# Performance work log

Measured on AMD Instinct MI355X. Metric: run time of the kernel, lower is better.

The kernel has to match this reference:

```python
import jax, jax.numpy as jnp
import numpy as np

N = 8192        # agents (single node type VEHICLE)
K = 15          # max_Nnode - 1 neighbors per node
E = N * K       # edges
FT = 12         # prediction horizon steps
SD = 4          # state dim (x, y, vx, vy)
ID = 2          # input dim (ax, ay)
ZD = 8          # latent z dim
HE = 256        # history_enc_dim
EE = 128        # edge_enc_dim
OH = 256        # obs_lstm_hidden_dim
GH = 256        # guide_RNN_hidden_dim
FH = 256        # FC_hidden_dim
AD = 16         # att_internal_dim
DT = 0.25
SCALE = 1.0     # input_scale


def setup_inputs() -> dict:
    ks = jax.random.split(jax.random.key(0), 40)
    f = lambda i, s: jax.random.normal(ks[i], s, jnp.float32)
    w = lambda i, s: 0.05 * jax.random.normal(ks[i], s, jnp.float32)
    inp = dict(
        x_last=f(0, (N, SD)), x_st_last=f(1, (N, SD)), hist_enc=f(2, (N, HE)),
        z=f(3, (N, ZD)),
        node_size=jax.random.uniform(ks[4], (N, 2), jnp.float32, 1.0, 3.0),
        W_h0=w(5, (SD, OH)), b_h0=w(6, (OH,)), W_c0=w(7, (SD, OH)), b_c0=w(8, (OH,)),
        W_gh=w(9, (HE + ZD, GH)), b_gh=w(10, (GH,)),
        W_gru_ih=w(11, (HE + ZD, 3 * GH)), W_gru_hh=w(12, (GH, 3 * GH)),
        b_gru_ih=w(13, (3 * GH,)), b_gru_hh=w(14, (3 * GH,)),
        W_proj=w(15, (GH, 2)), b_proj=w(16, (2,)),
        W_att1=w(17, (EE, AD)), W_att2=w(18, (SD, AD)), v_att=w(19, (AD,)),
        W_lstm_ih=w(20, (EE, 4 * OH)), W_lstm_hh=w(21, (OH, 4 * OH)),
        b_lstm_ih=w(22, (4 * OH,)), b_lstm_hh=w(23, (4 * OH,)),
        W_e1=w(24, (SD + 4, FH)), b_e1=w(25, (FH,)), W_e2=w(26, (FH, EE)), b_e2=w(27, (EE,)),
        W_a1=w(28, (OH + ZD + SD + 4, FH)), b_a1=w(29, (FH,)),
        W_a2=w(30, (FH, ID)), b_a2=w(31, (ID,)),
    )
    # edge k is the j-th neighbor of node k // K; index 0 in the enc table is the pad row
    inp["edge_idx1"] = jnp.repeat(jnp.arange(N), K)
    inp["edge_idx2"] = jax.random.randint(ks[32], (E,), 0, N)
    inp["node_obs_idx"] = (jnp.arange(E) + 1).reshape(N, K)
    inp["ft"] = FT
    return inp


def _dyn(s, u):
    # double-integrator: s = [x, y, vx, vy], u = [ax, ay]
    pos = s[:, :2] + s[:, 2:4] * DT + 0.5 * u * DT * DT
    vel = s[:, 2:4] + u * DT
    return jnp.concatenate([pos, vel], -1)


def _forward(x_last, x_st_last, hist_enc, z, node_size,
             W_h0, b_h0, W_c0, b_c0, W_gh, b_gh, W_gru_ih, W_gru_hh, b_gru_ih, b_gru_hh,
             W_proj, b_proj, W_att1, W_att2, v_att, W_lstm_ih, W_lstm_hh, b_lstm_ih, b_lstm_hh,
             W_e1, b_e1, W_e2, b_e2, W_a1, b_a1, W_a2, b_a2,
             edge_idx1, edge_idx2, node_obs_idx, ft):
    n = x_last.shape[0]
    ee = W_e2.shape[1]
    # ---- guide GRU: desired trajectory [ft, N, 2] ----
    xz = jnp.concatenate([hist_enc, z], -1)
    h0g = xz @ W_gh + b_gh
    gi = xz @ W_gru_ih + b_gru_ih  # input is constant over time (xz repeated)
    ir, iz, inn = jnp.split(gi, 3, -1)

    def gru_step(h, _):
        hr, hz, hn = jnp.split(h @ W_gru_hh + b_gru_hh, 3, -1)
        r = jax.nn.sigmoid(ir + hr)
        u = jax.nn.sigmoid(iz + hz)
        nh = (1.0 - u) * jnp.tanh(inn + r * hn) + u * h
        return nh, nh

    _, hs = jax.lax.scan(gru_step, h0g, None, length=ft)
    des = hs @ W_proj + b_proj                       # [ft, N, 2]
    des_next = jnp.concatenate([des[1:], des[-1:]], 0)
    des_prev = jnp.concatenate([jnp.zeros_like(des[:1]), des[:-1]], 0)
    first = jnp.zeros((ft,), jnp.float32).at[0].set(1.0)

    # ---- obs LSTM initial state ----
    h0 = x_st_last @ W_h0 + b_h0
    c0 = x_st_last @ W_c0 + b_c0

    size1 = node_size[edge_idx1]
    size2 = node_size[edge_idx2]
    rad = 0.5 * (jnp.linalg.norm(size1, axis=-1) + jnp.linalg.norm(size2, axis=-1))

    def step(carry, xs):
        prev, prev_st, h, c, terr, ccost = carry
        des_t, des_n, des_p, fst = xs
        # edge gather + collision cost + edge encoding
        s1 = prev[edge_idx1]
        s2 = prev[edge_idx2]
        dist = jnp.linalg.norm(s1[:, :2] - s2[:, :2], axis=-1)
        ccost = ccost + jnp.sum(jax.nn.relu(rad - dist))
        feat = jnp.concatenate([s2 - s1, size1, size2], -1)          # [E, SD+4]
        enc = jax.nn.relu(feat @ W_e1 + b_e1) @ W_e2 + b_e2          # [E, EE]
        enc_all = jnp.concatenate([jnp.zeros((1, ee), enc.dtype), enc], 0)
        obs = enc_all[node_obs_idx]                                   # [N, K, EE]
        # relative state (t==0 uses standardized history directly)
        m = 1.0 - fst
        rel = prev_st - m * x_st_last
        rel = jnp.concatenate([rel[:, :2] - m * des_p, rel[:, 2:]], -1)
        terr = terr + jnp.linalg.norm(rel[:, :2]) / n
        next_wp = des_t - prev_st[:, :2]
        next_wp2 = des_n - prev_st[:, :2]
        # additive attention over neighbors
        scores = jnp.tanh(obs @ W_att1 + (rel @ W_att2)[:, None, :]) @ v_att   # [N, K]
        att = jax.nn.softmax(scores, axis=-1)
        ctx = jnp.einsum('nk,nkd->nd', att, obs)
        # LSTM cell (torch gate order i, f, g, o)
        gates = ctx @ W_lstm_ih + b_lstm_ih + h @ W_lstm_hh + b_lstm_hh
        g_i, g_f, g_g, g_o = jnp.split(gates, 4, -1)
        c = jax.nn.sigmoid(g_f) * c + jax.nn.sigmoid(g_i) * jnp.tanh(g_g)
        h = jax.nn.sigmoid(g_o) * jnp.tanh(c)
        # action net + dynamics rollout
        a_in = jnp.concatenate([h, z, rel, next_wp, next_wp2], -1)   # [N, OH+ZD+SD+4]
        u = SCALE * jnp.tanh(jax.nn.relu(a_in @ W_a1 + b_a1) @ W_a2 + b_a2)
        nxt = _dyn(prev, u)
        nxt_st = _dyn(prev_st, u)
        return (nxt, nxt_st, h, c, terr, ccost), (nxt, u)

    zero = jnp.zeros((), jnp.float32)
    init = (x_last, x_st_last, h0, c0, zero, zero)
    (_, _, _, _, terr, ccost), (state_pred, input_pred) = jax.lax.scan(
        step, init, (des, des_next, des_prev, first))
    return state_pred, input_pred, terr, ccost


def reference(x_last, x_st_last, hist_enc, z, node_size,
              W_h0, b_h0, W_c0, b_c0, W_gh, b_gh, W_gru_ih, W_gru_hh, b_gru_ih, b_gru_hh,
              W_proj, b_proj, W_att1, W_att2, v_att, W_lstm_ih, W_lstm_hh, b_lstm_ih, b_lstm_hh,
              W_e1, b_e1, W_e2, b_e2, W_a1, b_a1, W_a2, b_a2,
              edge_idx1, edge_idx2, node_obs_idx, ft):
    return _forward(x_last, x_st_last, hist_enc, z, node_size,
                    W_h0, b_h0, W_c0, b_c0, W_gh, b_gh, W_gru_ih, W_gru_hh, b_gru_ih, b_gru_hh,
                    W_proj, b_proj, W_att1, W_att2, v_att, W_lstm_ih, W_lstm_hh, b_lstm_ih, b_lstm_hh,
                    W_e1, b_e1, W_e2, b_e2, W_a1, b_a1, W_a2, b_a2,
                    edge_idx1, edge_idx2, node_obs_idx, ft)
```

## Files before the change

### kernel.cpp

```cpp
#include <hip/hip_runtime.h>

#define DEVI __device__ __forceinline__

constexpr int N_  = 8192;
constexpr int K_  = 15;
constexpr int E_  = N_ * K_;
constexpr int FTS = 12;
constexpr float DT_ = 0.25f;

typedef __attribute__((ext_vector_type(8))) short short8x;
typedef __attribute__((ext_vector_type(4))) float float4x;

union U8 { unsigned int u[4]; short8x v; };

DEVI float sigf(float x) { return 1.0f / (1.0f + __expf(-x)); }
DEVI float tanhf_fast(float x) { float e = __expf(2.f * x); return 1.f - 2.f / (e + 1.f); }
DEVI unsigned int f2u(float x) { union { float f; unsigned int u; } c; c.f = x; return c.u; }
DEVI float u2f(unsigned int x) { union { unsigned int u; float f; } c; c.u = x; return c.f; }

DEVI void split8(const float* __restrict__ s, short8x& hi8, short8x& lo8) {
  U8 ph, pl;
#pragma unroll
  for (int p = 0; p < 4; p++) {
    float a0 = s[2*p], a1 = s[2*p+1];
    unsigned int u0 = f2u(a0), u1 = f2u(a1);
    unsigned int h0 = u0 & 0xFFFF0000u, h1 = u1 & 0xFFFF0000u;
    ph.u[p] = (u0 >> 16) | h1;
    float l0 = a0 - u2f(h0), l1 = a1 - u2f(h1);
    pl.u[p] = (f2u(l0) >> 16) | (f2u(l1) & 0xFFFF0000u);
  }
  hi8 = ph.v; lo8 = pl.v;
}

__global__ void k_zero(float* ss) {
  ss[blockIdx.x * 256 + threadIdx.x] = 0.f;
}

__global__ __launch_bounds__(256) void k_init_des(const float* __restrict__ b_proj,
                                                  float* __restrict__ des) {
  int i = blockIdx.x * 256 + threadIdx.x;
  des[i*2]     = b_proj[0];
  des[i*2 + 1] = b_proj[1];
}

__global__ __launch_bounds__(256) void k_edge_static(
    const int* __restrict__ e1, const int* __restrict__ e2,
    const float* __restrict__ nsize, float* __restrict__ rad, float* __restrict__ szf)
{
  int e = blockIdx.x * 256 + threadIdx.x;
  if (e >= E_) return;
  int i1 = e1[e], i2 = e2[e];
  float s1x = nsize[i1*2+0], s1y = nsize[i1*2+1];
  float s2x = nsize[i2*2+0], s2y = nsize[i2*2+1];
  rad[e] = 0.5f * (sqrtf(s1x*s1x + s1y*s1y) + sqrtf(s2x*s2x + s2y*s2y));
  *(float4*)&szf[e*4] = make_float4(s1x, s1y, s2x, s2y);
}

__global__ __launch_bounds__(256) void k_prep_hi(
    const float* __restrict__ W, unsigned short* __restrict__ out)
{
  int t = blockIdx.x * 256 + threadIdx.x;
  int fid = t >> 6, L = t & 63;
  int ks = fid >> 3, nt = fid & 7;
  int k0 = ks * 32 + (L >> 4) * 8;
  int n  = nt * 16 + (L & 15);
  unsigned int hi[4];
#pragma unroll
  for (int p = 0; p < 4; p++) {
    float w0 = W[(size_t)(k0 + 2*p) * 128 + n];
    float w1 = W[(size_t)(k0 + 2*p + 1) * 128 + n];
    hi[p] = (f2u(w0) >> 16) | (f2u(w1) & 0xFFFF0000u);
  }
  *(uint4*)(out + (size_t)fid * 512 + (size_t)L * 8) = make_uint4(hi[0], hi[1], hi[2], hi[3]);
}

__global__ __launch_bounds__(256) void k_prep1(
    const float* __restrict__ WA, const float* __restrict__ WB,
    int mode, int split, int wA, int wB, int Ktot, int NT, int nfrag,
    unsigned short* __restrict__ out)
{
  int t = blockIdx.x * 256 + threadIdx.x;
  int fid = t >> 6, L = t & 63;
  if (fid >= nfrag) return;
  int ks = fid / NT, nt = fid % NT;
  int k0 = ks * 32 + (L >> 4) * 8;
  int n  = nt * 16 + (L & 15);
  unsigned int hi[4];
#pragma unroll
  for (int p = 0; p < 4; p++) {
    float w0 = 0.f, w1 = 0.f;
    int ka = k0 + 2*p, kb = ka + 1;
    if (mode == 0) {
      if (ka < Ktot) w0 = (ka < split) ? WA[(size_t)ka*wA + n] : WB[(size_t)(ka-split)*wB + n];
      if (kb < Ktot) w1 = (kb < split) ? WA[(size_t)kb*wA + n] : WB[(size_t)(kb-split)*wB + n];
    } else {
      if (ka < Ktot) w0 = (n < split) ? WA[(size_t)ka*wA + n] : WB[(size_t)ka*wB + (n-split)];
      if (kb < Ktot) w1 = (n < split) ? WA[(size_t)kb*wA + n] : WB[(size_t)kb*wB + (n-split)];
    }
    hi[p] = (f2u(w0) >> 16) | (f2u(w1) & 0xFFFF0000u);
  }
  *(uint4*)(out + (size_t)fid * 512 + (size_t)L * 8) = make_uint4(hi[0], hi[1], hi[2], hi[3]);
}

__global__ __launch_bounds__(256) void k_xz_mfma(
    const float* __restrict__ hist, const float* __restrict__ z,
    const unsigned short* __restrict__ wB,
    const float* __restrict__ b_gh, const float* __restrict__ b_gih,
    float* __restrict__ gh0, float* __restrict__ gi)
{
  __shared__ __align__(16) float Abuf[2][64][36];
  const int tid = threadIdx.x;
  const int w = tid >> 6, lane = tid & 63;
  const int m = lane & 15, q = lane >> 4;
  const int n0 = blockIdx.x * 64;
  const int r_ = tid >> 2, c_ = (tid & 3) * 8;
  float4x acc[16];
#pragma unroll
  for (int tl = 0; tl < 16; tl++) acc[tl] = (float4x){0.f,0.f,0.f,0.f};

  auto LD = [&](int ks, float4& v0, float4& v1) {
    int kk = ks*32 + c_;
    int n = n0 + r_;
    if (kk < 256) {
      v0 = *(const float4*)&hist[(size_t)n*256 + kk];
      v1 = *(const float4*)&hist[(size_t)n*256 + kk + 4];
    } else if (kk == 256) {
      v0 = *(const float4*)&z[n*8];
      v1 = *(const float4*)&z[n*8 + 4];
    } else {
      v0 = make_float4(0,0,0,0); v1 = v0;
    }
  };
  {
    float4 v0, v1; LD(0, v0, v1);
    *(float4*)&Abuf[0][r_][c_]     = v0;
    *(float4*)&Abuf[0][r_][c_ + 4] = v1;
  }
  __syncthreads();
  for (int ks = 0; ks < 9; ks++) {
    float4 v0, v1;
    if (ks < 8) LD(ks + 1, v0, v1);
    short8x aHi, aLo;
    split8(&Abuf[ks & 1][w*16 + m][q*8], aHi, aLo);
#pragma unroll
    for (int tl = 0; tl < 16; tl++) {
      int nt = blockIdx.y*16 + tl;
      size_t off = (size_t)(ks*64 + nt) * 512 + (size_t)lane*8;
      short8x bh = *(const short8x*)(wB + off);
      acc[tl] = __builtin_amdgcn_mfma_f32_16x16x32_bf16(aLo, bh, acc[tl], 0, 0, 0);
      acc[tl] = __builtin_amdgcn_mfma_f32_16x16x32_bf16(aHi, bh, acc[tl], 0, 0, 0);
    }
    if (ks < 8) {
      *(float4*)&Abuf[(ks+1) & 1][r_][c_]     = v0;
      *(float4*)&Abuf[(ks+1) & 1][r_][c_ + 4] = v1;
      __syncthreads();
    }
  }
#pragma unroll
  for (int tl = 0; tl < 16; tl++) {
    int col = (blockIdx.y*16 + tl)*16 + m;
    float bias = (col < 256) ? b_gh[col] : b_gih[col - 256];
#pragma unroll
    for (int i = 0; i < 4; i++) {
      int n = n0 + w*16 + q*4 + i;
      float v = acc[tl][i] + bias;
      if (col < 256) gh0[(size_t)n*256 + col] = v;
      else           gi[(size_t)n*768 + col - 256] = v;
    }
  }
}

DEVI void gru_core(int tid, int n0, int j0,
                   const float* __restrict__ h_in, const unsigned short* __restrict__ wB,
                   const float* __restrict__ b_hh, const float* __restrict__ gi,
                   const float* __restrict__ W_proj, float* __restrict__ des_t,
                   float* __restrict__ h_out)
{
  const int w = tid >> 6, lane = tid & 63;
  const int m = lane & 15, q = lane >> 4;
  const float* __restrict__ hrow = h_in + (size_t)(n0 + w*16 + m) * 256 + q*8;
  float4x acc[12];
#pragma unroll
  for (int tl = 0; tl < 12; tl++) acc[tl] = (float4x){0.f,0.f,0.f,0.f};

  for (int ks = 0; ks < 8; ks++) {
    float a8[8];
    {
      float4 v0 = *(const float4*)(hrow + ks*32);
      float4 v1 = *(const float4*)(hrow + ks*32 + 4);
      a8[0]=v0.x; a8[1]=v0.y; a8[2]=v0.z; a8[3]=v0.w;
      a8[4]=v1.x; a8[5]=v1.y; a8[6]=v1.z; a8[7]=v1.w;
    }
    short8x aHi, aLo;
    split8(a8, aHi, aLo);
#pragma unroll
    for (int tl = 0; tl < 12; tl++) {
      int g = tl >> 2, jt = tl & 3;
      int nt = g*16 + (j0 >> 4) + jt;
      size_t off = (size_t)(ks*48 + nt) * 512 + (size_t)lane*8;
      short8x bh = *(const short8x*)(wB + off);
      acc[tl] = __builtin_amdgcn_mfma_f32_16x16x32_bf16(aLo, bh, acc[tl], 0, 0, 0);
      acc[tl] = __builtin_amdgcn_mfma_f32_16x16x32_bf16(aHi, bh, acc[tl], 0, 0, 0);
    }
  }
  float pd0[4] = {0,0,0,0}, pd1[4] = {0,0,0,0};
#pragma unroll
  for (int jt = 0; jt < 4; jt++) {
    int j = j0 + jt*16 + m;
    float br = b_hh[j], bz = b_hh[256 + j], bn = b_hh[512 + j];
    float wp0 = W_proj[j*2], wp1 = W_proj[j*2 + 1];
#pragma unroll
    for (int i = 0; i < 4; i++) {
      int n = n0 + w*16 + q*4 + i;
      float ir  = gi[(size_t)n*768 + j];
      float iz  = gi[(size_t)n*768 + 256 + j];
      float inn = gi[(size_t)n*768 + 512 + j];
      float hold = h_in[(size_t)n*256 + j];
      float r = sigf(ir + acc[0*4 + jt][i] + br);
      float u = sigf(iz + acc[1*4 + jt][i] + bz);
      float nh = (1.f - u) * tanhf_fast(inn + r * (acc[2*4 + jt][i] + bn)) + u * hold;
      h_out[(size_t)n*256 + j] = nh;
      pd0[i] += nh * wp0;
      pd1[i] += nh * wp1;
    }
  }
#pragma unroll
  for (int off = 1; off < 16; off <<= 1) {
#pragma unroll
    for (int i = 0; i < 4; i++) {
      pd0[i] += __shfl_xor(pd0[i], off);
      pd1[i] += __shfl_xor(pd1[i], off);
    }
  }
  if (m == 0) {
#pragma unroll
    for (int i = 0; i < 4; i++) {
      int n = n0 + w*16 + q*4 + i;
      atomicAdd(&des_t[n*2],     pd0[i]);
      atomicAdd(&des_t[n*2 + 1], pd1[i]);
    }
  }
}

__global__ __launch_bounds__(256) void k_gru_mfma(
    const float* __restrict__ h_in, const unsigned short* __restrict__ wB,
    const float* __restrict__ b_hh, const float* __restrict__ gi,
    const float* __restrict__ W_proj, float* __restrict__ des_t,
    float* __restrict__ h_out)
{
  gru_core(threadIdx.x, blockIdx.x * 64, blockIdx.y * 64,
           h_in, wB, b_hh, gi, W_proj, des_t, h_out);
}

__global__ __launch_bounds__(256) void k_lstm_mfma(
    const float* __restrict__ ctxg, const float* __restrict__ h_in,
    const unsigned short* __restrict__ wB,
    const float* __restrict__ b_ih, const float* __restrict__ b_hh,
    float* __restrict__ c_st, float* __restrict__ h_out)
{
  __shared__ __align__(16) float Abuf[2][64][36];
  const int tid = threadIdx.x;
  const int w = tid >> 6, lane = tid & 63;
  const int m = lane & 15, q = lane >> 4;
  const int n0 = blockIdx.x * 64;
  const int j0 = blockIdx.y * 32;
  const int r_ = tid >> 2, c_ = (tid & 3) * 8;
  float4x acc[8];
#pragma unroll
  for (int tl = 0; tl < 8; tl++) acc[tl] = (float4x){0.f,0.f,0.f,0.f};

  auto LD = [&](int ks, float4& v0, float4& v1) {
    int kk = ks*32 + c_;
    int n = n0 + r_;
    if (kk < 128) {
      v0 = *(const float4*)&ctxg[(size_t)n*128 + kk];
      v1 = *(const float4*)&ctxg[(size_t)n*128 + kk + 4];
    } else {
      v0 = *(const float4*)&h_in[(size_t)n*256 + kk - 128];
      v1 = *(const float4*)&h_in[(size_t)n*256 + kk - 124];
    }
  };
  {
    float4 v0, v1; LD(0, v0, v1);
    *(float4*)&Abuf[0][r_][c_]     = v0;
    *(float4*)&Abuf[0][r_][c_ + 4] = v1;
  }
  __syncthreads();
  for (int ks = 0; ks < 12; ks++) {
    float4 v0, v1;
    if (ks < 11) LD(ks + 1, v0, v1);
    short8x aHi, aLo;
    split8(&Abuf[ks & 1][w*16 + m][q*8], aHi, aLo);
#pragma unroll
    for (int tl = 0; tl < 8; tl++) {
      int g = tl >> 1, jt = tl & 1;
      int nt = g*16 + (j0 >> 4) + jt;
      size_t off = (size_t)(ks*64 + nt) * 512 + (size_t)lane*8;
      short8x bh = *(const short8x*)(wB + off);
      acc[tl] = __builtin_amdgcn_mfma_f32_16x16x32_bf16(aLo, bh, acc[tl], 0, 0, 0);
      acc[tl] = __builtin_amdgcn_mfma_f32_16x16x32_bf16(aHi, bh, acc[tl], 0, 0, 0);
    }
    if (ks < 11) {
      *(float4*)&Abuf[(ks+1) & 1][r_][c_]     = v0;
      *(float4*)&Abuf[(ks+1) & 1][r_][c_ + 4] = v1;
      __syncthreads();
    }
  }
#pragma unroll
  for (int jt = 0; jt < 2; jt++) {
    int j = j0 + jt*16 + m;
    float bi = b_ih[j]       + b_hh[j];
    float bf = b_ih[256 + j] + b_hh[256 + j];
    float bg = b_ih[512 + j] + b_hh[512 + j];
    float bo = b_ih[768 + j] + b_hh[768 + j];
#pragma unroll
    for (int i = 0; i < 4; i++) {
      int n = n0 + w*16 + q*4 + i;
      float g_i = sigf(acc[0*2 + jt][i] + bi);
      float g_f = sigf(acc[1*2 + jt][i] + bf);
      float g_g = tanhf_fast(acc[2*2 + jt][i] + bg);
      float g_o = sigf(acc[3*2 + jt][i] + bo);
      float cv = g_f * c_st[(size_t)n*256 + j] + g_i * g_g;
      c_st[(size_t)n*256 + j] = cv;
      h_out[(size_t)n*256 + j] = g_o * tanhf_fast(cv);
    }
  }
}

__global__ __launch_bounds__(256) void k_action_mfma(
    const float* __restrict__ h, const float* __restrict__ z,
    const float* __restrict__ rel, const float* __restrict__ nwp, const float* __restrict__ nwp2,
    const unsigned short* __restrict__ wB, const float* __restrict__ b_a1,
    const float* __restrict__ W_a2, const float* __restrict__ b_a2,
    float* __restrict__ prev, float* __restrict__ prev_st,
    float* __restrict__ outS, float* __restrict__ outU)
{
  __shared__ __align__(16) float Abuf[2][32][36];
  __shared__ float sm_p[2][16][2];
  const int tid = threadIdx.x;
  const int w = tid >> 6, lane = tid & 63;
  const int m = lane & 15, q = lane >> 4;
  const int ng = w >> 1, hh = w & 1;
  const int n0 = blockIdx.x * 32;
  const int r_ = tid >> 3, c_ = (tid & 7) * 4;
  float4x acc[8];
#pragma unroll
  for (int j = 0; j < 8; j++) acc[j] = (float4x){0.f,0.f,0.f,0.f};

  auto LD = [&](int ks) -> float4 {
    int kk = ks*32 + c_;
    int n = n0 + r_;
    float4 v;
    if (kk < 256)       v = *(const float4*)&h[(size_t)n*256 + kk];
    else if (kk == 256) v = *(const float4*)&z[n*8];
    else if (kk == 260) v = *(const float4*)&z[n*8 + 4];
    else if (kk == 264) v = *(const float4*)&rel[n*4];
    else if (kk == 268) {
      float2 w1 = *(const float2*)&nwp[n*2];
      float2 w2 = *(const float2*)&nwp2[n*2];
      v = make_float4(w1.x, w1.y, w2.x, w2.y);
    } else v = make_float4(0,0,0,0);
    return v;
  };
  {
    float4 v = LD(0);
    *(float4*)&Abuf[0][r_][c_] = v;
  }
  __syncthreads();
  for (int ks = 0; ks < 9; ks++) {
    float4 v;
    if (ks < 8) v = LD(ks + 1);
    short8x aHi, aLo;
    split8(&Abuf[ks & 1][ng*16 + m][q*8], aHi, aLo);
#pragma unroll
    for (int j = 0; j < 8; j++) {
      int tl = hh*8 + j;
      size_t off = (size_t)(ks*16 + tl) * 512 + (size_t)lane*8;
      short8x bh = *(const short8x*)(wB + off);
      acc[j] = __builtin_amdgcn_mfma_f32_16x16x32_bf16(aLo, bh, acc[j], 0, 0, 0);
      acc[j] = __builtin_amdgcn_mfma_f32_16x16x32_bf16(aHi, bh, acc[j], 0, 0, 0);
    }
    if (ks < 8) {
      *(float4*)&Abuf[(ks+1) & 1][r_][c_] = v;
      __syncthreads();
    }
  }
  float p0[4] = {0,0,0,0}, p1[4] = {0,0,0,0};
#pragma unroll
  for (int j = 0; j < 8; j++) {
    int col = (hh*8 + j)*16 + m;
    float ba = b_a1[col];
    float2 w2 = *(const float2*)&W_a2[col*2];
#pragma unroll
    for (int i = 0; i < 4; i++) {
      float hv = fmaxf(acc[j][i] + ba, 0.f);
      p0[i] += hv * w2.x;
      p1[i] += hv * w2.y;
    }
  }
#pragma unroll
  for (int off = 1; off < 16; off <<= 1) {
#pragma unroll
    for (int i = 0; i < 4; i++) {
      p0[i] += __shfl_xor(p0[i], off);
      p1[i] += __shfl_xor(p1[i], off);
    }
  }
  if (hh == 1 && m == 0) {
#pragma unroll
    for (int i = 0; i < 4; i++) {
      sm_p[ng][q*4 + i][0] = p0[i];
      sm_p[ng][q*4 + i][1] = p1[i];
    }
  }
  __syncthreads();
  if (hh == 0 && m == 0) {
    float ba0 = b_a2[0], ba1 = b_a2[1];
    const float hd = 0.5f * DT_ * DT_;
#pragma unroll
    for (int i = 0; i < 4; i++) {
      int n = n0 + ng*16 + q*4 + i;
      float ux = tanhf_fast(p0[i] + sm_p[ng][q*4 + i][0] + ba0);
      float uy = tanhf_fast(p1[i] + sm_p[ng][q*4 + i][1] + ba1);
      float4 pv = *(const float4*)&prev[n*4];
      float4 ps = *(const float4*)&prev_st[n*4];
      float4 npv, nps;
      npv.x = pv.x + pv.z*DT_ + ux*hd;
      npv.y = pv.y + pv.w*DT_ + uy*hd;
      npv.z = pv.z + ux*DT_;
      npv.w = pv.w + uy*DT_;
      nps.x = ps.x + ps.z*DT_ + ux*hd;
      nps.y = ps.y + ps.w*DT_ + uy*hd;
      nps.z = ps.z + ux*DT_;
      nps.w = ps.w + uy*DT_;
      *(float4*)&prev[n*4] = npv;
      *(float4*)&prev_st[n*4] = nps;
      *(float4*)&outS[(size_t)n*4] = npv;
      outU[n*2]     = ux;
      outU[n*2 + 1] = uy;
    }
  }
}

__global__ __launch_bounds__(256) void k_init_hc(
    const float* __restrict__ x_last, const float* __restrict__ x_st_last,
    const float* __restrict__ W_h0, const float* __restrict__ b_h0,
    const float* __restrict__ W_c0, const float* __restrict__ b_c0,
    float* __restrict__ h, float* __restrict__ c,
    float* __restrict__ prev, float* __restrict__ prev_st)
{
  const int n = blockIdx.x;
  const int j = threadIdx.x;
  float x0 = x_st_last[n*4], x1 = x_st_last[n*4+1], x2 = x_st_last[n*4+2], x3 = x_st_last[n*4+3];
  h[(size_t)n*256 + j] = b_h0[j] + x0*W_h0[j] + x1*W_h0[256+j] + x2*W_h0[512+j] + x3*W_h0[768+j];
  c[(size_t)n*256 + j] = b_c0[j] + x0*W_c0[j] + x1*W_c0[256+j] + x2*W_c0[512+j] + x3*W_c0[768+j];
  if (j < 4) prev[n*4 + j] = x_last[n*4 + j];
  else if (j < 8) prev_st[n*4 + (j-4)] = x_st_last[n*4 + (j-4)];
}

__global__ __launch_bounds__(256, 4) void k_edge_gru(
    const float* __restrict__ prev, const float* __restrict__ prev_st,
    const float* __restrict__ x_st_last,
    const float* __restrict__ szf, const float* __restrict__ rad,
    const int* __restrict__ nobs, const int* __restrict__ e1, const int* __restrict__ e2,
    const float* __restrict__ W_e1, const float* __restrict__ b_e1,
    const unsigned short* __restrict__ wsB, const float* __restrict__ b_e2,
    const unsigned short* __restrict__ wattA, const float* __restrict__ W_att2,
    const float* __restrict__ v_att,
    const float* __restrict__ des_p, const float* __restrict__ des_t,
    const float* __restrict__ des_n,
    float* __restrict__ relg, float* __restrict__ nwp, float* __restrict__ nwp2,
    float* __restrict__ ctx, float* __restrict__ ss_t, float* __restrict__ cc,
    const float* __restrict__ g_hin, const unsigned short* __restrict__ wBg,
    const float* __restrict__ b_ghh, const float* __restrict__ gi,
    const float* __restrict__ W_proj, float* __restrict__ des_g,
    float* __restrict__ g_hout, int gru_on)
{
  __shared__ __align__(16) float smem[4776];
  const int tid = threadIdx.x;
  const int bid = blockIdx.x;

  if ((bid % 5) == 4) {
    if (!gru_on) return;
    int b = bid / 5;
    gru_core(tid, (b & 127) * 64, (b >> 7) * 64,
             g_hin, wBg, b_ghh, gi, W_proj, des_g, g_hout);
    return;
  }
  const int eb = bid - (bid + 1) / 5;

  float* sm_stage = smem;
  float* sm_feats = smem + 4096;
  float* sm_flags = smem + 4608;
  float* sm_relv  = smem + 4672;
  float* sm_watt2 = smem + 4688;
  float* sm_vatt  = smem + 4752;
  float* sm_red   = smem + 4768;

  const int n0  = eb * 4;
  const int slot = (eb & 15) << 4;
  const int lane = tid & 63;
  const int g    = tid >> 6;
  const int q = lane >> 4, m = lane & 15;

  if (tid >= 176 && tid < 192) sm_vatt[tid - 176] = v_att[tid - 176];
  if (tid >= 192) sm_watt2[tid - 192] = W_att2[tid - 192];

  if (tid < 64) {
    float v = 0.f;
    if (tid < 60) {
      int gg = tid / 15, k = tid % 15;
      int idx = nobs[(n0 + gg) * 15 + k];
      float f[8] = {0,0,0,0,0,0,0,0};
      float fl = 0.f;
      if (idx > 0) {
        int e = idx - 1;
        int i1 = e1[e], i2 = e2[e];
#pragma unroll
        for (int d = 0; d < 4; d++) f[d] = prev[i2*4 + d] - prev[i1*4 + d];
        float4 sz = *(const float4*)&szf[(size_t)e*4];
        f[4] = sz.x; f[5] = sz.y; f[6] = sz.z; f[7] = sz.w;
        fl = 1.f;
        float dist = sqrtf(f[0]*f[0] + f[1]*f[1]);
        v = fmaxf(rad[e] - dist, 0.f);
      }
#pragma unroll
      for (int d = 0; d < 8; d++) sm_feats[(gg*16 + k)*8 + d] = f[d];
      sm_flags[gg*16 + k] = fl;
    } else {
      int gg = tid - 60;
#pragma unroll
      for (int d = 0; d < 8; d++) sm_feats[(gg*16 + 15)*8 + d] = 0.f;
      sm_flags[gg*16 + 15] = 0.f;
    }
#pragma unroll
    for (int off = 32; off; off >>= 1) v += __shfl_down(v, off);
    if (tid == 0) atomicAdd(cc + slot, v);
  } else if (tid < 68) {
    int gg = tid - 64;
    int n = n0 + gg;
    float4 ps = *(const float4*)&prev_st[n*4];
    float r0, r1, r2, r3;
    if (des_p) {
      float4 xs = *(const float4*)&x_st_last[n*4];
      r0 = ps.x - xs.x - des_p[n*2];
      r1 = ps.y - xs.y - des_p[n*2 + 1];
      r2 = ps.z - xs.z;
      r3 = ps.w - xs.w;
    } else { r0 = ps.x; r1 = ps.y; r2 = ps.z; r3 = ps.w; }
    sm_relv[gg*4+0] = r0; sm_relv[gg*4+1] = r1; sm_relv[gg*4+2] = r2; sm_relv[gg*4+3] = r3;
    *(float4*)&relg[n*4] = make_float4(r0, r1, r2, r3);
    nwp[n*2]      = des_t[n*2]     - ps.x;
    nwp[n*2 + 1]  = des_t[n*2 + 1] - ps.y;
    nwp2[n*2]     = des_n[n*2]     - ps.x;
    nwp2[n*2 + 1] = des_n[n*2 + 1] - ps.y;
    sm_red[gg] = r0*r0 + r1*r1;
  }
  {
    const uint4* src = (const uint4*)wsB;
    uint4* dst = (uint4*)sm_stage;
    dst[tid]       = src[tid];
    dst[tid + 256] = src[tid + 256];
  }
  __syncthreads();
  if (tid == 64) atomicAdd(ss_t + slot, sm_red[0] + sm_red[1] + sm_red[2] + sm_red[3]);

  float f[8];
  {
    const float4 fa = *(const float4*)&sm_feats[(g*16 + m)*8];
    const float4 fb = *(const float4*)&sm_feats[(g*16 + m)*8 + 4];
    f[0]=fa.x; f[1]=fa.y; f[2]=fa.z; f[3]=fa.w; f[4]=fb.x; f[5]=fb.y; f[6]=fb.z; f[7]=fb.w;
  }
  float4x encR[8];
#pragma unroll
  for (int nt = 0; nt < 8; nt++) encR[nt] = (float4x){0.f,0.f,0.f,0.f};
  const float4* We14 = (const float4*)W_e1;
  const float4* Be14 = (const float4*)b_e1;

  for (int ks = 0; ks < 8; ks++) {
    uint4 r0, r1;
    if (ks < 7) {
      const uint4* src = (const uint4*)wsB + (ks + 1) * 512;
      r0 = src[tid];
      r1 = src[tid + 256];
    }
    short8x aHi, aLo;
    {
      float h8[8];
      float4 b0 = Be14[8*ks + 2*q];
      float4 b1 = Be14[8*ks + 2*q + 1];
      h8[0]=b0.x; h8[1]=b0.y; h8[2]=b0.z; h8[3]=b0.w; h8[4]=b1.x; h8[5]=b1.y; h8[6]=b1.z; h8[7]=b1.w;
#pragma unroll
      for (int d = 0; d < 8; d++) {
        float4 wa = We14[d*64 + ks*8 + 2*q];
        float4 wb = We14[d*64 + ks*8 + 2*q + 1];
        h8[0] += f[d]*wa.x; h8[1] += f[d]*wa.y; h8[2] += f[d]*wa.z; h8[3] += f[d]*wa.w;
        h8[4] += f[d]*wb.x; h8[5] += f[d]*wb.y; h8[6] += f[d]*wb.z; h8[7] += f[d]*wb.w;
      }
#pragma unroll
      for (int p = 0; p < 8; p++) h8[p] = fmaxf(h8[p], 0.f);
      split8(h8, aHi, aLo);
    }
    const unsigned short* sb = (const unsigned short*)sm_stage + (ks & 1) * 4096;
#pragma unroll
    for (int nt = 0; nt < 8; nt++) {
      short8x bh = *(const short8x*)(sb + nt*512 + lane*8);
      encR[nt] = __builtin_amdgcn_mfma_f32_16x16x32_bf16(aLo, bh, encR[nt], 0, 0, 0);
      encR[nt] = __builtin_amdgcn_mfma_f32_16x16x32_bf16(aHi, bh, encR[nt], 0, 0, 0);
    }
    if (ks < 7) {
      uint4* dst = (uint4*)sm_stage + ((ks + 1) & 1) * 512;
      dst[tid]       = r0;
      dst[tid + 256] = r1;
      __syncthreads();
    }
  }
  float4x fl4 = *(const float4x*)&sm_flags[g*16 + q*4];
#pragma unroll
  for (int nt = 0; nt < 8; nt++) {
    float b2 = b_e2[nt*16 + m];
#pragma unroll
    for (int i = 0; i < 4; i++) encR[nt][i] = (encR[nt][i] + b2) * fl4[i];
  }

  __syncthreads();
  {
  }
  float* tb = sm_stage + g * 576;
  float4x sacc = {0.f, 0.f, 0.f, 0.f};
#pragma unroll
  for (int ksc = 0; ksc < 4; ksc++) {
#pragma unroll
    for (int ntl = 0; ntl < 2; ntl++) {
#pragma unroll
      for (int i = 0; i < 4; i++)
        tb[(q*4 + i)*36 + ntl*16 + m] = encR[2*ksc + ntl][i];
    }
    __builtin_amdgcn_s_waitcnt(0);
    float a8[8];
    {
      const float4* tp = (const float4*)(tb + m*36 + q*8);
      float4 t0 = tp[0], t1 = tp[1];
      a8[0]=t0.x; a8[1]=t0.y; a8[2]=t0.z; a8[3]=t0.w;
      a8[4]=t1.x; a8[5]=t1.y; a8[6]=t1.z; a8[7]=t1.w;
    }
    __builtin_amdgcn_s_waitcnt(0);
    short8x aH, aL;
    split8(a8, aH, aL);
    short8x bh = *(const short8x*)(wattA + ksc*512 + lane*8);
    sacc = __builtin_amdgcn_mfma_f32_16x16x32_bf16(aL, bh, sacc, 0, 0, 0);
    sacc = __builtin_amdgcn_mfma_f32_16x16x32_bf16(aH, bh, sacc, 0, 0, 0);
  }

  float relw;
  {
    float4 rv = *(const float4*)&sm_relv[g*4];
    relw = rv.x * sm_watt2[m] + rv.y * sm_watt2[16 + m]
         + rv.z * sm_watt2[32 + m] + rv.w * sm_watt2[48 + m];
  }
  float vat = sm_vatt[m];
  float val[4];
#pragma unroll
  for (int i = 0; i < 4; i++) val[i] = tanhf_fast(sacc[i] + relw) * vat;
#pragma unroll
  for (int msk = 1; msk < 16; msk <<= 1) {
#pragma unroll
    for (int i = 0; i < 4; i++) val[i] += __shfl_xor(val[i], msk);
  }
  if (q == 3) val[3] = -3.0e38f;
  float mx = fmaxf(fmaxf(val[0], val[1]), fmaxf(val[2], val[3]));
  mx = fmaxf(mx, __shfl_xor(mx, 16));
  mx = fmaxf(mx, __shfl_xor(mx, 32));
  float4x ev;
  float ssum = 0.f;
#pragma unroll
  for (int i = 0; i < 4; i++) { ev[i] = __expf(val[i] - mx); ssum += ev[i]; }
  ssum += __shfl_xor(ssum, 16);
  ssum += __shfl_xor(ssum, 32);
  float inv = 1.f / ssum;
#pragma unroll
  for (int i = 0; i < 4; i++) ev[i] *= inv;

  float cpart[8];
#pragma unroll
  for (int nt = 0; nt < 8; nt++) {
    float cv = ev[0]*encR[nt][0] + ev[1]*encR[nt][1] + ev[2]*encR[nt][2] + ev[3]*encR[nt][3];
    cv += __shfl_xor(cv, 16);
    cv += __shfl_xor(cv, 32);
    cpart[nt] = cv;
  }
  float v0 = (q == 0) ? cpart[0] : (q == 1) ? cpart[2] : (q == 2) ? cpart[4] : cpart[6];
  float v1 = (q == 0) ? cpart[1] : (q == 1) ? cpart[3] : (q == 2) ? cpart[5] : cpart[7];
  size_t cb = (size_t)(n0 + g) * 128 + q*32 + m;
  ctx[cb]      = v0;
  ctx[cb + 16] = v1;
}

__global__ void k_final(const float* __restrict__ ss, float* __restrict__ out) {
  const int lane = threadIdx.x;
  float red[13];
#pragma unroll
  for (int a = 0; a < 13; a++) {
    float v = (lane < 16) ? ss[a*256 + lane*16] : 0.f;
    v += __shfl_xor(v, 1);
    v += __shfl_xor(v, 2);
    v += __shfl_xor(v, 4);
    v += __shfl_xor(v, 8);
    red[a] = v;
  }
  if (lane == 0) {
    float t = 0.f;
    for (int i = 0; i < FTS; i++) t += sqrtf(red[i]);
    out[(size_t)FTS * N_ * 6]     = t / (float)N_;
    out[(size_t)FTS * N_ * 6 + 1] = red[12];
  }
}

extern "C" void kernel_launch(void* const* d_in, const int* in_sizes, int n_in,
                              void* d_out, int out_size, void* d_ws, size_t ws_size,
                              hipStream_t stream) {
  (void)in_sizes; (void)n_in; (void)out_size;
  const float* x_last    = (const float*)d_in[0];
  const float* x_st_last = (const float*)d_in[1];
  const float* hist_enc  = (const float*)d_in[2];
  const float* z         = (const float*)d_in[3];
  const float* node_size = (const float*)d_in[4];
  const float* W_h0 = (const float*)d_in[5];
  const float* b_h0 = (const float*)d_in[6];
  const float* W_c0 = (const float*)d_in[7];
  const float* b_c0 = (const float*)d_in[8];
  const float* W_gh = (const float*)d_in[9];
  const float* b_gh = (const float*)d_in[10];
  const float* W_gih = (const float*)d_in[11];
  const float* W_ghh = (const float*)d_in[12];
  const float* b_gih = (const float*)d_in[13];
  const float* b_ghh = (const float*)d_in[14];
  const float* W_proj = (const float*)d_in[15];
  const float* b_proj = (const float*)d_in[16];
  const float* W_att1 = (const float*)d_in[17];
  const float* W_att2 = (const float*)d_in[18];
  const float* v_att  = (const float*)d_in[19];
  const float* W_lih = (const float*)d_in[20];
  const float* W_lhh = (const float*)d_in[21];
  const float* b_lih = (const float*)d_in[22];
  const float* b_lhh = (const float*)d_in[23];
  const float* W_e1 = (const float*)d_in[24];
  const float* b_e1 = (const float*)d_in[25];
  const float* W_e2 = (const float*)d_in[26];
  const float* b_e2 = (const float*)d_in[27];
  const float* W_a1 = (const float*)d_in[28];
  const float* b_a1 = (const float*)d_in[29];
  const float* W_a2 = (const float*)d_in[30];
  const float* b_a2 = (const float*)d_in[31];
  const int* e1   = (const int*)d_in[32];
  const int* e2   = (const int*)d_in[33];
  const int* nobs = (const int*)d_in[34];
  float* out = (float*)d_out;

  float* wsf     = (float*)d_ws;
  float* prev    = wsf;
  float* prev_st = wsf + 32768;
  float* des     = wsf + 65536;
  float* rad     = wsf + 262160;
  float* szf     = wsf + 385040;
  float* baseA   = wsf + 876560;
  float* gh0 = baseA;
  float* gh1 = baseA + (size_t)N_ * 256;
  float* gi  = baseA + (size_t)2 * N_ * 256;
  float* hA   = baseA;
  float* hB   = baseA + (size_t)N_ * 256;
  float* cbuf = baseA + (size_t)2 * N_ * 256;
  float* ctx  = baseA + (size_t)3 * N_ * 256;
  float* rel  = baseA + (size_t)4 * N_ * 256;
  float* nwp  = rel + (size_t)N_ * 4;
  float* nwp2 = nwp + (size_t)N_ * 2;
  unsigned short* wsBe = (unsigned short*)(wsf + 11362320);
  unsigned short* wsBg = (unsigned short*)(wsf + 11427856);
  unsigned short* wsBl = (unsigned short*)(wsf + 11624464);
  unsigned short* wsBx = (unsigned short*)(wsf + 12017680);
  unsigned short* wsBa = (unsigned short*)(wsf + 12312592);
  unsigned short* wattA = (unsigned short*)(wsf + 12386320);
  float* ssx = wsf + 12388368;
  float* ext = wsf + 12391696;
  const size_t needF = 12391696ull + 5ull * N_ * 256ull;
  const bool fuse = ws_size >= needF * 4ull;
  float* gh0F = fuse ? ext : gh0;
  float* gh1F = fuse ? (ext + (size_t)N_ * 256) : gh1;
  float* giF  = fuse ? (ext + (size_t)2 * N_ * 256) : gi;

  k_zero<<<13, 256, 0, stream>>>(ssx);
  k_edge_static<<<(E_ + 255) / 256, 256, 0, stream>>>(e1, e2, node_size, rad, szf);
  k_init_des<<<FTS * N_ / 256, 256, 0, stream>>>(b_proj, des);

  k_prep_hi<<<16, 256, 0, stream>>>(W_e2, wsBe);
  k_prep1<<<96,  256, 0, stream>>>(W_ghh, W_ghh, 0, 256, 768,  768,  256, 48, 384, wsBg);
  k_prep1<<<192, 256, 0, stream>>>(W_lih, W_lhh, 0, 128, 1024, 1024, 384, 64, 768, wsBl);
  k_prep1<<<144, 256, 0, stream>>>(W_gh,  W_gih, 1, 256, 256,  768,  264, 64, 576, wsBx);
  k_prep1<<<36,  256, 0, stream>>>(W_a1,  W_a1,  0, 272, 256,  256,  272, 16, 144, wsBa);
  k_prep1<<<1,   256, 0, stream>>>(W_att1, W_att1, 0, 128, 16, 16, 128, 1, 4, wattA);

  k_xz_mfma<<<dim3(128, 4), 256, 0, stream>>>(hist_enc, z, wsBx, b_gh, b_gih, gh0F, giF);
  const int pre = fuse ? 2 : FTS;
  float* gcur = gh0F;
  float* gnxt = gh1F;
  for (int t = 0; t < pre; t++) {
    k_gru_mfma<<<dim3(128, 4), 256, 0, stream>>>(gcur, wsBg, b_ghh, giF, W_proj,
                                                 des + (size_t)t * N_ * 2, gnxt);
    float* tmp = gcur; gcur = gnxt; gnxt = tmp;
  }

  k_init_hc<<<N_, 256, 0, stream>>>(x_last, x_st_last, W_h0, b_h0, W_c0, b_c0,
                                    hA, cbuf, prev, prev_st);
  float* hcur = hA;
  float* hnxt = hB;
  for (int t = 0; t < FTS; t++) {
    const float* des_t = des + (size_t)t * N_ * 2;
    const float* des_n = des + (size_t)((t + 1 < FTS) ? t + 1 : FTS - 1) * N_ * 2;
    const float* des_p = (t > 0) ? des + (size_t)(t - 1) * N_ * 2 : nullptr;
    const int gs = t + 2;
    const int gru_on = (fuse && gs < FTS) ? 1 : 0;
    const float* gin = (gs & 1) ? gh1F : gh0F;
    float* gout      = (gs & 1) ? gh0F : gh1F;
    float* des_g = des + (size_t)((gs < FTS) ? gs : 0) * N_ * 2;
    k_edge_gru<<<2560, 256, 0, stream>>>(prev, prev_st, x_st_last, szf, rad,
                                         nobs, e1, e2, W_e1, b_e1, wsBe, b_e2,
                                         wattA, W_att2, v_att,
                                         des_p, des_t, des_n,
                                         rel, nwp, nwp2, ctx,
                                         ssx + (size_t)t * 256, ssx + 12 * 256,
                                         gin, wsBg, b_ghh, giF, W_proj, des_g, gout, gru_on);
    k_lstm_mfma<<<dim3(128, 8), 256, 0, stream>>>(ctx, hcur, wsBl, b_lih, b_lhh,
                                                  cbuf, hnxt);
    k_action_mfma<<<256, 256, 0, stream>>>(hnxt, z, rel, nwp, nwp2,
                                           wsBa, b_a1, W_a2, b_a2,
                                           prev, prev_st,
                                           out + (size_t)t * N_ * 4,
                                           out + (size_t)FTS * N_ * 4 + (size_t)t * N_ * 2);
    float* tmp = hcur; hcur = hnxt; hnxt = tmp;
  }
  k_final<<<1, 64, 0, stream>>>(ssx, out);
}
```

Measured before the change: 1.525 ms.

## Run all GRU steps in one persistent kernel with hidden state in LDS

Replaces the per-step GRU launches, previously partly interleaved into the edge kernel, with a single kernel. Each block owns 32 nodes and runs all 12 steps, keeping the hidden state double-buffered in shared memory, and reduces the projection in LDS instead of using atomics. The r and z input gates are stored as packed bf16, which halves their traffic but lowers precision. The edge kernel no longer carries GRU blocks, so the overlap between the GRU and the first edge steps is lost. Only 256 blocks of 512 threads run the serial GRU chain.

```diff
diff --git a/kernel.cpp b/kernel.cpp
--- a/kernel.cpp
+++ b/kernel.cpp
@@ -34,13 +34,6 @@
 
 __global__ void k_zero(float* ss) {
   ss[blockIdx.x * 256 + threadIdx.x] = 0.f;
-}
-
-__global__ __launch_bounds__(256) void k_init_des(const float* __restrict__ b_proj,
-                                                  float* __restrict__ des) {
-  int i = blockIdx.x * 256 + threadIdx.x;
-  des[i*2]     = b_proj[0];
-  des[i*2 + 1] = b_proj[1];
 }
 
 __global__ __launch_bounds__(256) void k_edge_static(
@@ -106,7 +99,8 @@
     const float* __restrict__ hist, const float* __restrict__ z,
     const unsigned short* __restrict__ wB,
     const float* __restrict__ b_gh, const float* __restrict__ b_gih,
-    float* __restrict__ gh0, float* __restrict__ gi)
+    float* __restrict__ gh0, unsigned int* __restrict__ gi_ru,
+    float* __restrict__ gi_n)
 {
   __shared__ __align__(16) float Abuf[2][64][36];
   const int tid = threadIdx.x;
@@ -164,92 +158,128 @@
     for (int i = 0; i < 4; i++) {
       int n = n0 + w*16 + q*4 + i;
       float v = acc[tl][i] + bias;
-      if (col < 256) gh0[(size_t)n*256 + col] = v;
-      else           gi[(size_t)n*768 + col - 256] = v;
-    }
-  }
-}
-
-DEVI void gru_core(int tid, int n0, int j0,
-                   const float* __restrict__ h_in, const unsigned short* __restrict__ wB,
-                   const float* __restrict__ b_hh, const float* __restrict__ gi,
-                   const float* __restrict__ W_proj, float* __restrict__ des_t,
-                   float* __restrict__ h_out)
+      if (col < 256) {
+        gh0[(size_t)n*256 + col] = v;
+      } else {
+        int cj = col - 256;
+        int gate = cj >> 8, j = cj & 255;
+        if (gate == 2) gi_n[(size_t)n*256 + j] = v;
+        else ((unsigned short*)gi_ru)[((size_t)n*256 + j)*2 + gate] =
+               (unsigned short)(f2u(v) >> 16);
+      }
+    }
+  }
+}
+
+__global__ __launch_bounds__(512) void k_gru_all(
+    const float* __restrict__ gh0, const unsigned short* __restrict__ wB,
+    const float* __restrict__ b_ghh,
+    const unsigned int* __restrict__ gi_ru, const float* __restrict__ gi_n,
+    const float* __restrict__ W_proj, const float* __restrict__ b_proj,
+    float* __restrict__ des)
 {
+  __shared__ __align__(16) float h_lds[2][32][260];
+  __shared__ float sm_des[4][32][2];
+  const int tid = threadIdx.x;
   const int w = tid >> 6, lane = tid & 63;
   const int m = lane & 15, q = lane >> 4;
-  const float* __restrict__ hrow = h_in + (size_t)(n0 + w*16 + m) * 256 + q*8;
-  float4x acc[12];
-#pragma unroll
-  for (int tl = 0; tl < 12; tl++) acc[tl] = (float4x){0.f,0.f,0.f,0.f};
-
-  for (int ks = 0; ks < 8; ks++) {
-    float a8[8];
-    {
-      float4 v0 = *(const float4*)(hrow + ks*32);
-      float4 v1 = *(const float4*)(hrow + ks*32 + 4);
-      a8[0]=v0.x; a8[1]=v0.y; a8[2]=v0.z; a8[3]=v0.w;
-      a8[4]=v1.x; a8[5]=v1.y; a8[6]=v1.z; a8[7]=v1.w;
-    }
-    short8x aHi, aLo;
-    split8(a8, aHi, aLo);
-#pragma unroll
-    for (int tl = 0; tl < 12; tl++) {
-      int g = tl >> 2, jt = tl & 3;
-      int nt = g*16 + (j0 >> 4) + jt;
-      size_t off = (size_t)(ks*48 + nt) * 512 + (size_t)lane*8;
-      short8x bh = *(const short8x*)(wB + off);
-      acc[tl] = __builtin_amdgcn_mfma_f32_16x16x32_bf16(aLo, bh, acc[tl], 0, 0, 0);
-      acc[tl] = __builtin_amdgcn_mfma_f32_16x16x32_bf16(aHi, bh, acc[tl], 0, 0, 0);
-    }
-  }
-  float pd0[4] = {0,0,0,0}, pd1[4] = {0,0,0,0};
+  const int rh = w & 1, jh = w >> 1;
+  const int n0 = blockIdx.x * 32;
+
+  {
+    int r = tid >> 4, c = (tid & 15) * 16;
+    const float4* src = (const float4*)&gh0[(size_t)(n0 + r)*256 + c];
+    float4 v0 = src[0], v1 = src[1], v2 = src[2], v3 = src[3];
+    *(float4*)&h_lds[0][r][c]      = v0;
+    *(float4*)&h_lds[0][r][c + 4]  = v1;
+    *(float4*)&h_lds[0][r][c + 8]  = v2;
+    *(float4*)&h_lds[0][r][c + 12] = v3;
+  }
+  float br_[4], bz_[4], bn_[4], wp0_[4], wp1_[4];
 #pragma unroll
   for (int jt = 0; jt < 4; jt++) {
-    int j = j0 + jt*16 + m;
-    float br = b_hh[j], bz = b_hh[256 + j], bn = b_hh[512 + j];
-    float wp0 = W_proj[j*2], wp1 = W_proj[j*2 + 1];
-#pragma unroll
-    for (int i = 0; i < 4; i++) {
-      int n = n0 + w*16 + q*4 + i;
-      float ir  = gi[(size_t)n*768 + j];
-      float iz  = gi[(size_t)n*768 + 256 + j];
-      float inn = gi[(size_t)n*768 + 512 + j];
-      float hold = h_in[(size_t)n*256 + j];
-      float r = sigf(ir + acc[0*4 + jt][i] + br);
-      float u = sigf(iz + acc[1*4 + jt][i] + bz);
-      float nh = (1.f - u) * tanhf_fast(inn + r * (acc[2*4 + jt][i] + bn)) + u * hold;
-      h_out[(size_t)n*256 + j] = nh;
-      pd0[i] += nh * wp0;
-      pd1[i] += nh * wp1;
-    }
-  }
-#pragma unroll
-  for (int off = 1; off < 16; off <<= 1) {
-#pragma unroll
-    for (int i = 0; i < 4; i++) {
-      pd0[i] += __shfl_xor(pd0[i], off);
-      pd1[i] += __shfl_xor(pd1[i], off);
-    }
-  }
-  if (m == 0) {
-#pragma unroll
-    for (int i = 0; i < 4; i++) {
-      int n = n0 + w*16 + q*4 + i;
-      atomicAdd(&des_t[n*2],     pd0[i]);
-      atomicAdd(&des_t[n*2 + 1], pd1[i]);
-    }
-  }
-}
-
-__global__ __launch_bounds__(256) void k_gru_mfma(
-    const float* __restrict__ h_in, const unsigned short* __restrict__ wB,
-    const float* __restrict__ b_hh, const float* __restrict__ gi,
-    const float* __restrict__ W_proj, float* __restrict__ des_t,
-    float* __restrict__ h_out)
-{
-  gru_core(threadIdx.x, blockIdx.x * 64, blockIdx.y * 64,
-           h_in, wB, b_hh, gi, W_proj, des_t, h_out);
+    int j = jh*64 + jt*16 + m;
+    br_[jt] = b_ghh[j];
+    bz_[jt] = b_ghh[256 + j];
+    bn_[jt] = b_ghh[512 + j];
+    wp0_[jt] = W_proj[j*2];
+    wp1_[jt] = W_proj[j*2 + 1];
+  }
+  const float bp0 = b_proj[0], bp1 = b_proj[1];
+  __syncthreads();
+
+  for (int t = 0; t < FTS; t++) {
+    float (*hc)[260] = h_lds[t & 1];
+    float (*hn)[260] = h_lds[(t + 1) & 1];
+    float4x acc[12];
+#pragma unroll
+    for (int tl = 0; tl < 12; tl++) acc[tl] = (float4x){0.f,0.f,0.f,0.f};
+
+#pragma unroll 2
+    for (int ks = 0; ks < 8; ks++) {
+      float a8[8];
+      {
+        const float* hp = &hc[rh*16 + m][ks*32 + q*8];
+        float4 v0 = *(const float4*)hp;
+        float4 v1 = *(const float4*)(hp + 4);
+        a8[0]=v0.x; a8[1]=v0.y; a8[2]=v0.z; a8[3]=v0.w;
+        a8[4]=v1.x; a8[5]=v1.y; a8[6]=v1.z; a8[7]=v1.w;
+      }
+      short8x aHi, aLo;
+      split8(a8, aHi, aLo);
+#pragma unroll
+      for (int tl = 0; tl < 12; tl++) {
+        int g = tl >> 2, jt = tl & 3;
+        int nt = g*16 + jh*4 + jt;
+        size_t off = (size_t)(ks*48 + nt) * 512 + (size_t)lane*8;
+        short8x bh = *(const short8x*)(wB + off);
+        acc[tl] = __builtin_amdgcn_mfma_f32_16x16x32_bf16(aLo, bh, acc[tl], 0, 0, 0);
+        acc[tl] = __builtin_amdgcn_mfma_f32_16x16x32_bf16(aHi, bh, acc[tl], 0, 0, 0);
+      }
+    }
+    float pd0[4] = {0,0,0,0}, pd1[4] = {0,0,0,0};
+#pragma unroll
+    for (int jt = 0; jt < 4; jt++) {
+      int j = jh*64 + jt*16 + m;
+#pragma unroll
+      for (int i = 0; i < 4; i++) {
+        int rl = rh*16 + q*4 + i;
+        unsigned int ru = gi_ru[(size_t)(n0 + rl)*256 + j];
+        float ir  = u2f(ru << 16);
+        float iz  = u2f(ru & 0xFFFF0000u);
+        float inn = gi_n[(size_t)(n0 + rl)*256 + j];
+        float hold = hc[rl][j];
+        float r = sigf(ir + acc[0*4 + jt][i] + br_[jt]);
+        float u = sigf(iz + acc[1*4 + jt][i] + bz_[jt]);
+        float nh = (1.f - u) * tanhf_fast(inn + r * (acc[2*4 + jt][i] + bn_[jt])) + u * hold;
+        hn[rl][j] = nh;
+        pd0[i] += nh * wp0_[jt];
+        pd1[i] += nh * wp1_[jt];
+      }
+    }
+#pragma unroll
+    for (int off = 1; off < 16; off <<= 1) {
+#pragma unroll
+      for (int i = 0; i < 4; i++) {
+        pd0[i] += __shfl_xor(pd0[i], off);
+        pd1[i] += __shfl_xor(pd1[i], off);
+      }
+    }
+    if (m == 0) {
+#pragma unroll
+      for (int i = 0; i < 4; i++) {
+        sm_des[jh][rh*16 + q*4 + i][0] = pd0[i];
+        sm_des[jh][rh*16 + q*4 + i][1] = pd1[i];
+      }
+    }
+    __syncthreads();
+    if (tid < 64) {
+      int r = tid >> 1, c = tid & 1;
+      float s = sm_des[0][r][c] + sm_des[1][r][c] + sm_des[2][r][c] + sm_des[3][r][c];
+      des[((size_t)t * N_ + n0 + r) * 2 + c] = s + (c ? bp1 : bp0);
+    }
+    __syncthreads();
+  }
 }
 
 __global__ __launch_bounds__(256) void k_lstm_mfma(
@@ -458,7 +488,7 @@
   else if (j < 8) prev_st[n*4 + (j-4)] = x_st_last[n*4 + (j-4)];
 }
 
-__global__ __launch_bounds__(256, 4) void k_edge_gru(
+__global__ __launch_bounds__(256, 4) void k_edge(
     const float* __restrict__ prev, const float* __restrict__ prev_st,
     const float* __restrict__ x_st_last,
     const float* __restrict__ szf, const float* __restrict__ rad,
@@ -470,24 +500,11 @@
     const float* __restrict__ des_p, const float* __restrict__ des_t,
     const float* __restrict__ des_n,
     float* __restrict__ relg, float* __restrict__ nwp, float* __restrict__ nwp2,
-    float* __restrict__ ctx, float* __restrict__ ss_t, float* __restrict__ cc,
-    const float* __restrict__ g_hin, const unsigned short* __restrict__ wBg,
-    const float* __restrict__ b_ghh, const float* __restrict__ gi,
-    const float* __restrict__ W_proj, float* __restrict__ des_g,
-    float* __restrict__ g_hout, int gru_on)
+    float* __restrict__ ctx, float* __restrict__ ss_t, float* __restrict__ cc)
 {
   __shared__ __align__(16) float smem[4776];
   const int tid = threadIdx.x;
-  const int bid = blockIdx.x;
-
-  if ((bid % 5) == 4) {
-    if (!gru_on) return;
-    int b = bid / 5;
-    gru_core(tid, (b & 127) * 64, (b >> 7) * 64,
-             g_hin, wBg, b_ghh, gi, W_proj, des_g, g_hout);
-    return;
-  }
-  const int eb = bid - (bid + 1) / 5;
+  const int eb = blockIdx.x;
 
   float* sm_stage = smem;
   float* sm_feats = smem + 4096;
@@ -719,7 +736,7 @@
 extern "C" void kernel_launch(void* const* d_in, const int* in_sizes, int n_in,
                               void* d_out, int out_size, void* d_ws, size_t ws_size,
                               hipStream_t stream) {
-  (void)in_sizes; (void)n_in; (void)out_size;
+  (void)in_sizes; (void)n_in; (void)out_size; (void)ws_size;
   const float* x_last    = (const float*)d_in[0];
   const float* x_st_last = (const float*)d_in[1];
   const float* hist_enc  = (const float*)d_in[2];
@@ -764,9 +781,9 @@
   float* rad     = wsf + 262160;
   float* szf     = wsf + 385040;
   float* baseA   = wsf + 876560;
-  float* gh0 = baseA;
-  float* gh1 = baseA + (size_t)N_ * 256;
-  float* gi  = baseA + (size_t)2 * N_ * 256;
+  float* gh0           = baseA;
+  unsigned int* gi_ru  = (unsigned int*)(baseA + (size_t)2 * N_ * 256);
+  float* gi_n          = baseA + (size_t)3 * N_ * 256;
   float* hA   = baseA;
   float* hB   = baseA + (size_t)N_ * 256;
   float* cbuf = baseA + (size_t)2 * N_ * 256;
@@ -781,16 +798,9 @@
   unsigned short* wsBa = (unsigned short*)(wsf + 12312592);
   unsigned short* wattA = (unsigned short*)(wsf + 12386320);
   float* ssx = wsf + 12388368;
-  float* ext = wsf + 12391696;
-  const size_t needF = 12391696ull + 5ull * N_ * 256ull;
-  const bool fuse = ws_size >= needF * 4ull;
-  float* gh0F = fuse ? ext : gh0;
-  float* gh1F = fuse ? (ext + (size_t)N_ * 256) : gh1;
-  float* giF  = fuse ? (ext + (size_t)2 * N_ * 256) : gi;
 
   k_zero<<<13, 256, 0, stream>>>(ssx);
   k_edge_static<<<(E_ + 255) / 256, 256, 0, stream>>>(e1, e2, node_size, rad, szf);
-  k_init_des<<<FTS * N_ / 256, 256, 0, stream>>>(b_proj, des);
 
   k_prep_hi<<<16, 256, 0, stream>>>(W_e2, wsBe);
   k_prep1<<<96,  256, 0, stream>>>(W_ghh, W_ghh, 0, 256, 768,  768,  256, 48, 384, wsBg);
@@ -799,15 +809,10 @@
   k_prep1<<<36,  256, 0, stream>>>(W_a1,  W_a1,  0, 272, 256,  256,  272, 16, 144, wsBa);
   k_prep1<<<1,   256, 0, stream>>>(W_att1, W_att1, 0, 128, 16, 16, 128, 1, 4, wattA);
 
-  k_xz_mfma<<<dim3(128, 4), 256, 0, stream>>>(hist_enc, z, wsBx, b_gh, b_gih, gh0F, giF);
-  const int pre = fuse ? 2 : FTS;
-  float* gcur = gh0F;
-  float* gnxt = gh1F;
-  for (int t = 0; t < pre; t++) {
-    k_gru_mfma<<<dim3(128, 4), 256, 0, stream>>>(gcur, wsBg, b_ghh, giF, W_proj,
-                                                 des + (size_t)t * N_ * 2, gnxt);
-    float* tmp = gcur; gcur = gnxt; gnxt = tmp;
-  }
+  k_xz_mfma<<<dim3(128, 4), 256, 0, stream>>>(hist_enc, z, wsBx, b_gh, b_gih,
+                                              gh0, gi_ru, gi_n);
+  k_gru_all<<<256, 512, 0, stream>>>(gh0, wsBg, b_ghh, gi_ru, gi_n,
+                                     W_proj, b_proj, des);
 
   k_init_hc<<<N_, 256, 0, stream>>>(x_last, x_st_last, W_h0, b_h0, W_c0, b_c0,
                                     hA, cbuf, prev, prev_st);
@@ -817,18 +822,12 @@
     const float* des_t = des + (size_t)t * N_ * 2;
     const float* des_n = des + (size_t)((t + 1 < FTS) ? t + 1 : FTS - 1) * N_ * 2;
     const float* des_p = (t > 0) ? des + (size_t)(t - 1) * N_ * 2 : nullptr;
-    const int gs = t + 2;
-    const int gru_on = (fuse && gs < FTS) ? 1 : 0;
-    const float* gin = (gs & 1) ? gh1F : gh0F;
-    float* gout      = (gs & 1) ? gh0F : gh1F;
-    float* des_g = des + (size_t)((gs < FTS) ? gs : 0) * N_ * 2;
-    k_edge_gru<<<2560, 256, 0, stream>>>(prev, prev_st, x_st_last, szf, rad,
-                                         nobs, e1, e2, W_e1, b_e1, wsBe, b_e2,
-                                         wattA, W_att2, v_att,
-                                         des_p, des_t, des_n,
-                                         rel, nwp, nwp2, ctx,
-                                         ssx + (size_t)t * 256, ssx + 12 * 256,
-                                         gin, wsBg, b_ghh, giF, W_proj, des_g, gout, gru_on);
+    k_edge<<<2048, 256, 0, stream>>>(prev, prev_st, x_st_last, szf, rad,
+                                     nobs, e1, e2, W_e1, b_e1, wsBe, b_e2,
+                                     wattA, W_att2, v_att,
+                                     des_p, des_t, des_n,
+                                     rel, nwp, nwp2, ctx,
+                                     ssx + (size_t)t * 256, ssx + 12 * 256);
     k_lstm_mfma<<<dim3(128, 8), 256, 0, stream>>>(ctx, hcur, wsBl, b_lih, b_lhh,
                                                   cbuf, hnxt);
     k_action_mfma<<<256, 256, 0, stream>>>(hnxt, z, rel, nwp, nwp2,
```

Result: faster. 1.479 ms (-3.0%).
